# Kernel tuning notes

Hardware: AMD Instinct MI355X
Metric: run time of the kernel (lower is better)

## Reference

```python
import jax, jax.numpy as jnp
import numpy as np

PAD_Y = 16
PAD_X = 16


def setup_inputs() -> dict:
    key = jax.random.key(0)
    k1, k2, k3, k4 = jax.random.split(key, 4)
    B, NLAM, H, W = 4, 96, 256, 256
    KS = 15
    cube = jax.random.normal(k1, (B, NLAM, H, W), dtype=jnp.float32)
    # per-(ksequence, wavelength) dispersion shifts in pixels (a few px)
    dx = 3.0 * jax.random.normal(k2, (4, NLAM), dtype=jnp.float32)
    dy = 3.0 * jax.random.normal(k3, (4, NLAM), dtype=jnp.float32)
    psf = jax.random.uniform(k4, (KS, KS), dtype=jnp.float32)
    psf = psf / psf.sum()  # normalised PSF as in the original
    return {"cube": cube, "dx": dx, "dy": dy, "psf_kernel": psf}


def _forward(cube, dx, dy, psf_kernel):
    B, n_lam, H, W = cube.shape
    H_out, W_out = H + 2 * PAD_Y, W + 2 * PAD_X
    padded = jnp.pad(cube, ((0, 0), (0, 0), (PAD_Y, PAD_Y), (PAD_X, PAD_X)))
    yy, xx = jnp.meshgrid(jnp.arange(H_out, dtype=cube.dtype),
                          jnp.arange(W_out, dtype=cube.dtype), indexing="ij")

    def shift_one(img_b, d_x, d_y):
        # img_b: (B, H_out, W_out); output[y,x] = input[y-dy, x-dx], bilinear,
        # zeros outside (matches grid_sample padding_mode='zeros', align_corners=True)
        coords = jnp.stack([yy - d_y, xx - d_x])  # (2, H_out, W_out)
        return jax.vmap(lambda im: jax.scipy.ndimage.map_coordinates(
            im, coords, order=1, mode="constant", cval=0.0))(img_b)

    def per_k(dxk, dyk):
        # vmap over wavelengths -> (n_lam, B, H_out, W_out); accumulate over lambda
        shifted = jax.vmap(shift_one, in_axes=(1, 0, 0))(padded, dxk, dyk)
        return shifted.sum(0)  # (B, H_out, W_out)

    acc = jax.vmap(per_k)(dx, dy)            # (4, B, H_out, W_out)
    acc = jnp.transpose(acc, (1, 0, 2, 3))   # (B, 4, H_out, W_out)

    # PSF conv (same kernel every channel); conv is linear so conv(sum) == sum(conv)
    ks = psf_kernel.shape[-1]
    p = ks // 2
    x = acc.reshape(B * 4, 1, H_out, W_out)
    kern = psf_kernel.reshape(1, 1, ks, ks)
    out = jax.lax.conv_general_dilated(
        x, kern, window_strides=(1, 1), padding=[(p, p), (p, p)],
        dimension_numbers=("NCHW", "OIHW", "NCHW"))
    return out.reshape(B, 4, H_out, W_out)


def reference(cube, dx, dy, psf_kernel):
    return _forward(cube, dx, dy, psf_kernel)
```

## Files before the change

### kernel.cpp

```cpp
#include <hip/hip_runtime.h>

#define BB 4
#define NLAM 96
#define HH 256
#define WW 256
#define HO 288
#define WO 288
#define NK 4
#define KS 15
#define PADK 7

#define ACC_N ((size_t)BB * NK * HO * WO)

#define SP 105
#define SROWS 65
#define SQUADS 26

typedef float f4 __attribute__((ext_vector_type(4), aligned(4)));
typedef float f4a __attribute__((ext_vector_type(4)));

__global__ __launch_bounds__(384) void params_k(const float* __restrict__ dx,
                                                const float* __restrict__ dy,
                                                float4* __restrict__ pw,
                                                int2* __restrict__ po,
                                                int4* __restrict__ gmm) {
    __shared__ int sox[384], soy[384];
    const int i = threadIdx.x;
    const float sx = -dx[i] - 16.0f;
    const float sy = -dy[i] - 16.0f;
    const float fx = floorf(sx), fy = floorf(sy);
    const int ox = (int)fx, oy = (int)fy;
    po[i] = make_int2(ox, oy);
    pw[i] = make_float4(1.0f - (sx - fx), sx - fx, 1.0f - (sy - fy), sy - fy);
    sox[i] = ox; soy[i] = oy;
    __syncthreads();
    if (i < 64) {
        int mnx = sox[i], mxx = mnx, mny = soy[i], mxy = mny;
        for (int j = i + 64; j < 384; j += 64) {
            mnx = min(mnx, sox[j]); mxx = max(mxx, sox[j]);
            mny = min(mny, soy[j]); mxy = max(mxy, soy[j]);
        }
        for (int m = 32; m; m >>= 1) {
            mnx = min(mnx, __shfl_xor(mnx, m, 64));
            mxx = max(mxx, __shfl_xor(mxx, m, 64));
            mny = min(mny, __shfl_xor(mny, m, 64));
            mxy = max(mxy, __shfl_xor(mxy, m, 64));
        }
        if (i == 0) *gmm = make_int4(mnx, mxx, mny, mxy);
    }
}

__global__ __launch_bounds__(256, 4) void shift_accum(
        const float* __restrict__ cube,
        const float4* __restrict__ pw,
        const int2* __restrict__ po,
        const int4* __restrict__ gmm,
        float* __restrict__ part,
        int S, int chunk) {
    __shared__ float tile[SROWS * SP];
    const int zc  = blockIdx.z;
    const int b   = zc / S;
    const int c   = zc - b * S;
    const int tx0 = blockIdx.x * 64;
    const int ty0 = blockIdx.y * 32;
    const int tx  = threadIdx.x, ty = threadIdx.y;
    const int x   = tx0 + tx * 4;
    const int y   = ty0 + ty * 2;
    const int tid = ty * 16 + tx;
    const float* __restrict__ cb = cube + (size_t)b * NLAM * HH * WW;

    const int4 mm = *gmm;
    const int spanX = mm.y - mm.x;
    const int spanY = mm.w - mm.z;
    const bool lds_ok = (spanX <= 32) && (spanY <= 31);

    f4 a[NK][2];
#pragma unroll
    for (int k = 0; k < NK; ++k) { a[k][0] = (f4)0.f; a[k][1] = (f4)0.f; }

    const int l0 = min(NLAM, c * chunk);
    const int l1 = min(NLAM, l0 + chunk);

    if (lds_ok) {
        const int row0 = ty0 + mm.z;
        const int col0 = (tx0 + mm.x) & ~3;
        const int R    = spanY + 34;
        const int lrb  = ty * 2 - mm.z;
        const int lcb  = tx * 4 + (tx0 - col0);

        for (int lam = l0; lam < l1; ++lam) {
            const float* __restrict__ img = cb + lam * (HH * WW);
            for (int q = tid; q < R * SQUADS; q += 256) {
                const int r  = q / SQUADS;
                const int qi = q - r * SQUADS;
                const int gy = row0 + r;
                const int gc = col0 + qi * 4;
                f4a v = {0.f, 0.f, 0.f, 0.f};
                if ((unsigned)gy < (unsigned)HH) {
                    const float* rp = img + (gy << 8);
                    if ((unsigned)gc <= (unsigned)(WW - 4)) {
                        v = *(const f4a*)(rp + gc);
                    } else {
#pragma unroll
                        for (int e = 0; e < 4; ++e)
                            if ((unsigned)(gc + e) < (unsigned)WW) v[e] = rp[gc + e];
                    }
                }
                const int la = r * SP + qi * 4;
                tile[la]     = v.x; tile[la + 1] = v.y;
                tile[la + 2] = v.z; tile[la + 3] = v.w;
            }
            __syncthreads();
#pragma unroll
            for (int k = 0; k < NK; ++k) {
                const int i_ = k * NLAM + lam;
                const int2 o = po[i_]; const float4 w = pw[i_];
                const float* t = &tile[(lrb + o.y) * SP + (lcb + o.x)];
                float t0[5], t1[5], t2[5];
#pragma unroll
                for (int cc = 0; cc < 5; ++cc) {
                    t0[cc] = t[cc];
                    t1[cc] = t[SP + cc];
                    t2[cc] = t[2 * SP + cc];
                }
                float vb0[5], vb1[5];
#pragma unroll
                for (int cc = 0; cc < 5; ++cc) {
                    vb0[cc] = w.z * t0[cc] + w.w * t1[cc];
                    vb1[cc] = w.z * t1[cc] + w.w * t2[cc];
                }
                f4 d0, d1;
                d0.x = w.x * vb0[0] + w.y * vb0[1];
                d0.y = w.x * vb0[1] + w.y * vb0[2];
                d0.z = w.x * vb0[2] + w.y * vb0[3];
                d0.w = w.x * vb0[3] + w.y * vb0[4];
                d1.x = w.x * vb1[0] + w.y * vb1[1];
                d1.y = w.x * vb1[1] + w.y * vb1[2];
                d1.z = w.x * vb1[2] + w.y * vb1[3];
                d1.w = w.x * vb1[3] + w.y * vb1[4];
                a[k][0] += d0; a[k][1] += d1;
            }
            __syncthreads();
        }
    } else {
        for (int lam = l0; lam < l1; ++lam) {
            const float* __restrict__ img = cb + lam * (HH * WW);
#pragma unroll
            for (int k = 0; k < NK; ++k) {
                const int i_ = k * NLAM + lam;
                const int2 o = po[i_]; const float4 w = pw[i_];
#pragma unroll
                for (int j = 0; j < 2; ++j) {
                    const int iy = y + j + o.y;
                    const int ix = x + o.x;
                    const int cy0 = min(max(iy, 0), HH - 1);
                    const int cy1 = min(max(iy + 1, 0), HH - 1);
                    const float my0 = ((unsigned)iy       < (unsigned)HH) ? w.z : 0.0f;
                    const float my1 = ((unsigned)(iy + 1) < (unsigned)HH) ? w.w : 0.0f;
                    const float* r0p = img + cy0 * WW;
                    const float* r1p = img + cy1 * WW;
                    float rb[5];
#pragma unroll
                    for (int cc = 0; cc < 5; ++cc) {
                        const int cx = min(max(ix + cc, 0), WW - 1);
                        const float m = ((unsigned)(ix + cc) < (unsigned)WW) ? 1.0f : 0.0f;
                        rb[cc] = m * (my0 * r0p[cx] + my1 * r1p[cx]);
                    }
                    f4 d;
                    d.x = w.x * rb[0] + w.y * rb[1];
                    d.y = w.x * rb[1] + w.y * rb[2];
                    d.z = w.x * rb[2] + w.y * rb[3];
                    d.w = w.x * rb[3] + w.y * rb[4];
                    a[k][j] += d;
                }
            }
        }
    }

    if (x < WO) {
        const size_t hw = (size_t)HO * WO;
        float* pa = part + (size_t)c * ACC_N + ((size_t)(b * NK) * HO + y) * WO + x;
#pragma unroll
        for (int k = 0; k < NK; ++k) {
            *(f4a*)(pa + (size_t)k * hw)      = a[k][0];
            *(f4a*)(pa + (size_t)k * hw + WO) = a[k][1];
        }
    }
}

#define TPX 112
template <int S>
__global__ __launch_bounds__(192) void conv_psf(const float* __restrict__ part,
                                                const float* __restrict__ psf,
                                                float* __restrict__ out) {
    __shared__ float tilec[46][TPX];
    __shared__ float spsf[KS * KS];
    const int bk  = blockIdx.z;
    const int gx0 = blockIdx.x * 96 - PADK;
    const int gy0 = blockIdx.y * 32 - PADK;
    const float* __restrict__ ap = part + (size_t)bk * HO * WO;

    const int tid = threadIdx.y * 24 + threadIdx.x;
    for (int i = tid; i < KS * KS; i += 192) spsf[i] = psf[i];
    for (int i = tid; i < 46 * 110; i += 192) {
        int r = i / 110, c = i - r * 110;
        int gy = gy0 + r, gx = gx0 + c;
        float v = 0.f;
        if ((unsigned)gy < (unsigned)HO && (unsigned)gx < (unsigned)WO) {
            const size_t idx = (size_t)gy * WO + gx;
            float t[S];
#pragma unroll
            for (int cc = 0; cc < S; ++cc)
                t[cc] = ap[(size_t)cc * ACC_N + idx];
#pragma unroll
            for (int cc = 0; cc < S; ++cc) v += t[cc];
        }
        tilec[r][c] = v;
    }
    __syncthreads();

    const int x0 = threadIdx.x * 4;
    const int y0 = threadIdx.y * 4;
    float o[4][4] = {};

    for (int rr = 0; rr < 18; ++rr) {
        const float* rp = &tilec[y0 + rr][x0];
        float row[18];
#pragma unroll
        for (int q = 0; q < 4; ++q) {
            f4a v = *(const f4a*)(rp + 4 * q);
            row[4 * q]     = v.x; row[4 * q + 1] = v.y;
            row[4 * q + 2] = v.z; row[4 * q + 3] = v.w;
        }
        row[16] = rp[16]; row[17] = rp[17];

#pragma unroll
        for (int j = 0; j < 4; ++j) {
            const int ky = rr - j;
            if (ky >= 0 && ky < KS) {
                const float* w = &spsf[ky * KS];
#pragma unroll
                for (int kx = 0; kx < KS; ++kx) {
                    const float wv = w[kx];
#pragma unroll
                    for (int i = 0; i < 4; ++i) o[j][i] += wv * row[kx + i];
                }
            }
        }
    }

    const int xo = blockIdx.x * 96 + x0;
    const int yo = blockIdx.y * 32 + y0;
    float* op = out + ((size_t)bk * HO + yo) * WO + xo;
#pragma unroll
    for (int j = 0; j < 4; ++j) {
        f4a v = { o[j][0], o[j][1], o[j][2], o[j][3] };
        *(f4a*)(op + (size_t)j * WO) = v;
    }
}

extern "C" void kernel_launch(void* const* d_in, const int* in_sizes, int n_in,
                              void* d_out, int out_size, void* d_ws, size_t ws_size,
                              hipStream_t stream) {
    const float* cube = (const float*)d_in[0];
    const float* dx   = (const float*)d_in[1];
    const float* dy   = (const float*)d_in[2];
    const float* psf  = (const float*)d_in[3];
    float* out = (float*)d_out;

    const size_t ACCB   = ACC_N * sizeof(float);
    const size_t tables = 384 * sizeof(float4) + 384 * sizeof(int2) + sizeof(int4);

    int S = 1;
    for (int cand : {8, 6, 5, 4, 3, 2}) {
        if (ws_size >= (size_t)cand * ACCB + tables) { S = cand; break; }
    }
    const int chunk = (NLAM + S - 1) / S;

    float* part = (float*)d_ws;
    char*  tb   = (char*)d_ws + (size_t)S * ACCB;
    float4* pw  = (float4*)tb;
    int2*   po  = (int2*)(tb + 384 * sizeof(float4));
    int4*   gmm = (int4*)(tb + 384 * sizeof(float4) + 384 * sizeof(int2));

    params_k<<<1, 384, 0, stream>>>(dx, dy, pw, po, gmm);

    dim3 b1(16, 16);
    dim3 g1((WO + 63) / 64, HO / 32, BB * S);
    shift_accum<<<g1, b1, 0, stream>>>(cube, pw, po, gmm, part, S, chunk);

    dim3 b2(24, 8);
    dim3 g2(WO / 96, HO / 32, BB * NK);
    switch (S) {
        case 8: conv_psf<8><<<g2, b2, 0, stream>>>(part, psf, out); break;
        case 6: conv_psf<6><<<g2, b2, 0, stream>>>(part, psf, out); break;
        case 5: conv_psf<5><<<g2, b2, 0, stream>>>(part, psf, out); break;
        case 4: conv_psf<4><<<g2, b2, 0, stream>>>(part, psf, out); break;
        case 3: conv_psf<3><<<g2, b2, 0, stream>>>(part, psf, out); break;
        case 2: conv_psf<2><<<g2, b2, 0, stream>>>(part, psf, out); break;
        default: conv_psf<1><<<g2, b2, 0, stream>>>(part, psf, out); break;
    }
}
```

Before: 255.6 us.

## Precompute tile-load addresses, vectorize bilinear math, retile PSF conv, raise split count

The shift kernel now computes per-thread global offsets, masks and LDS addresses for the tile load once, outside the wavelength loop. Edge handling becomes branchless masked vector loads with a rare partial-quad fallback, and the bilinear blend uses packed float4 arithmetic. The conv kernel switches to 16-row tiles with 2 output rows per thread, vectorized reduction of the partials and padded PSF rows read as float4, and the wavelength split can now go up to 12 partial buffers. This aims to cut integer and address overhead and improve occupancy, at the cost of more registers and more partial-buffer traffic when S is larger.

Measured after the change: 226.7 us. -11.3%, faster.

```diff
diff --git a/kernel.cpp b/kernel.cpp
--- a/kernel.cpp
+++ b/kernel.cpp
@@ -13,8 +13,9 @@
 #define ACC_N ((size_t)BB * NK * HO * WO)
 
 #define SP 105
-#define SROWS 65
-#define SQUADS 26
+#define TILE_N (65 * SP)
+#define SDUMMY TILE_N
+#define NQ 7
 
 typedef float f4 __attribute__((ext_vector_type(4), aligned(4)));
 typedef float f4a __attribute__((ext_vector_type(4)));
@@ -57,7 +58,7 @@
         const int4* __restrict__ gmm,
         float* __restrict__ part,
         int S, int chunk) {
-    __shared__ float tile[SROWS * SP];
+    __shared__ float tile[TILE_N + 8];
     const int zc  = blockIdx.z;
     const int b   = zc / S;
     const int c   = zc - b * S;
@@ -74,9 +75,9 @@
     const int spanY = mm.w - mm.z;
     const bool lds_ok = (spanX <= 32) && (spanY <= 31);
 
-    f4 a[NK][2];
-#pragma unroll
-    for (int k = 0; k < NK; ++k) { a[k][0] = (f4)0.f; a[k][1] = (f4)0.f; }
+    f4a a[NK][2];
+#pragma unroll
+    for (int k = 0; k < NK; ++k) { a[k][0] = (f4a)0.f; a[k][1] = (f4a)0.f; }
 
     const int l0 = min(NLAM, c * chunk);
     const int l1 = min(NLAM, l0 + chunk);
@@ -85,37 +86,70 @@
         const int row0 = ty0 + mm.z;
         const int col0 = (tx0 + mm.x) & ~3;
         const int R    = spanY + 34;
-        const int lrb  = ty * 2 - mm.z;
-        const int lcb  = tx * 4 + (tx0 - col0);
+        const int tb0  = (ty * 2 - mm.z) * SP + (tx * 4 + (tx0 - col0));
+
+        int  goffB[NQ];
+        int  waddr[NQ];
+        float mf[NQ];
+        int  pf = 0;
+#pragma unroll
+        for (int s = 0; s < NQ; ++s) {
+            const int q  = tid + s * 256;
+            const bool inR = q < R * 26;
+            const int r  = q / 26;
+            const int qi = q - r * 26;
+            const int gy = row0 + r;
+            const int gc = col0 + qi * 4;
+            const bool rowOK = (unsigned)gy < (unsigned)HH;
+            const bool fullQ = rowOK && gc >= 0 && gc <= WW - 4;
+            const bool partQ = inR && rowOK && !fullQ && (gc + 3 >= 0) && (gc < WW);
+            const int gyc = min(max(gy, 0), HH - 1);
+            const int gcc = min(max(gc, 0), WW - 4);
+            goffB[s] = (gyc * WW + gcc) * 4;
+            mf[s]    = (inR && fullQ) ? 1.0f : 0.0f;
+            waddr[s] = (inR && !partQ) ? (r * SP + qi * 4) : SDUMMY;
+            if (partQ) pf |= 1 << s;
+        }
+
+        for (int i = tid; i < TILE_N + 8; i += 256) tile[i] = 0.0f;
+        __syncthreads();
 
         for (int lam = l0; lam < l1; ++lam) {
-            const float* __restrict__ img = cb + lam * (HH * WW);
-            for (int q = tid; q < R * SQUADS; q += 256) {
-                const int r  = q / SQUADS;
-                const int qi = q - r * SQUADS;
-                const int gy = row0 + r;
-                const int gc = col0 + qi * 4;
-                f4a v = {0.f, 0.f, 0.f, 0.f};
-                if ((unsigned)gy < (unsigned)HH) {
-                    const float* rp = img + (gy << 8);
-                    if ((unsigned)gc <= (unsigned)(WW - 4)) {
-                        v = *(const f4a*)(rp + gc);
-                    } else {
+            const char* __restrict__ ib = (const char*)(cb + lam * (HH * WW));
+#pragma unroll
+            for (int s = 0; s < NQ; ++s) {
+                f4a v = *(const f4a*)(ib + goffB[s]);
+                const float m = mf[s];
+                const int wa = waddr[s];
+                tile[wa]     = v.x * m;
+                tile[wa + 1] = v.y * m;
+                tile[wa + 2] = v.z * m;
+                tile[wa + 3] = v.w * m;
+            }
+            if (pf) {
+#pragma unroll
+                for (int s = 0; s < NQ; ++s) {
+                    if (pf & (1 << s)) {
+                        const int q  = tid + s * 256;
+                        const int r  = q / 26;
+                        const int qi = q - r * 26;
+                        const int gy = row0 + r;
+                        const int gc = col0 + qi * 4;
+                        const float* rp = (const float*)ib + gy * WW;
+                        const int la = r * SP + qi * 4;
 #pragma unroll
                         for (int e = 0; e < 4; ++e)
-                            if ((unsigned)(gc + e) < (unsigned)WW) v[e] = rp[gc + e];
+                            if ((unsigned)(gc + e) < (unsigned)WW)
+                                tile[la + e] = rp[gc + e];
                     }
                 }
-                const int la = r * SP + qi * 4;
-                tile[la]     = v.x; tile[la + 1] = v.y;
-                tile[la + 2] = v.z; tile[la + 3] = v.w;
             }
             __syncthreads();
 #pragma unroll
             for (int k = 0; k < NK; ++k) {
                 const int i_ = k * NLAM + lam;
                 const int2 o = po[i_]; const float4 w = pw[i_];
-                const float* t = &tile[(lrb + o.y) * SP + (lcb + o.x)];
+                const float* t = tile + tb0 + o.y * SP + o.x;
                 float t0[5], t1[5], t2[5];
 #pragma unroll
                 for (int cc = 0; cc < 5; ++cc) {
@@ -123,22 +157,17 @@
                     t1[cc] = t[SP + cc];
                     t2[cc] = t[2 * SP + cc];
                 }
-                float vb0[5], vb1[5];
-#pragma unroll
-                for (int cc = 0; cc < 5; ++cc) {
-                    vb0[cc] = w.z * t0[cc] + w.w * t1[cc];
-                    vb1[cc] = w.z * t1[cc] + w.w * t2[cc];
-                }
-                f4 d0, d1;
-                d0.x = w.x * vb0[0] + w.y * vb0[1];
-                d0.y = w.x * vb0[1] + w.y * vb0[2];
-                d0.z = w.x * vb0[2] + w.y * vb0[3];
-                d0.w = w.x * vb0[3] + w.y * vb0[4];
-                d1.x = w.x * vb1[0] + w.y * vb1[1];
-                d1.y = w.x * vb1[1] + w.y * vb1[2];
-                d1.z = w.x * vb1[2] + w.y * vb1[3];
-                d1.w = w.x * vb1[3] + w.y * vb1[4];
-                a[k][0] += d0; a[k][1] += d1;
+                f4a r0 = {t0[0], t0[1], t0[2], t0[3]};
+                f4a r1 = {t1[0], t1[1], t1[2], t1[3]};
+                f4a r2 = {t2[0], t2[1], t2[2], t2[3]};
+                f4a vb0 = w.z * r0 + w.w * r1;
+                f4a vb1 = w.z * r1 + w.w * r2;
+                const float e0 = w.z * t0[4] + w.w * t1[4];
+                const float e1 = w.z * t1[4] + w.w * t2[4];
+                f4a s0 = {vb0.y, vb0.z, vb0.w, e0};
+                f4a s1 = {vb1.y, vb1.z, vb1.w, e1};
+                a[k][0] += w.x * vb0 + w.y * s0;
+                a[k][1] += w.x * vb1 + w.y * s1;
             }
             __syncthreads();
         }
@@ -166,7 +195,7 @@
                         const float m = ((unsigned)(ix + cc) < (unsigned)WW) ? 1.0f : 0.0f;
                         rb[cc] = m * (my0 * r0p[cx] + my1 * r1p[cx]);
                     }
-                    f4 d;
+                    f4a d;
                     d.x = w.x * rb[0] + w.y * rb[1];
                     d.y = w.x * rb[1] + w.y * rb[2];
                     d.z = w.x * rb[2] + w.y * rb[3];
@@ -188,43 +217,74 @@
     }
 }
 
-#define TPX 112
+#define CPX 112
+#define CROWS 30
+#define CTILE_N (CROWS * CPX)
+#define CDUMMY CTILE_N
+#define NQC 5
+
 template <int S>
 __global__ __launch_bounds__(192) void conv_psf(const float* __restrict__ part,
                                                 const float* __restrict__ psf,
                                                 float* __restrict__ out) {
-    __shared__ float tilec[46][TPX];
-    __shared__ float spsf[KS * KS];
+    __shared__ float tilec[CTILE_N + 8];
+    __shared__ float spsf[KS][16];
     const int bk  = blockIdx.z;
     const int gx0 = blockIdx.x * 96 - PADK;
-    const int gy0 = blockIdx.y * 32 - PADK;
+    const int gy0 = blockIdx.y * 16 - PADK;
     const float* __restrict__ ap = part + (size_t)bk * HO * WO;
 
     const int tid = threadIdx.y * 24 + threadIdx.x;
-    for (int i = tid; i < KS * KS; i += 192) spsf[i] = psf[i];
-    for (int i = tid; i < 46 * 110; i += 192) {
-        int r = i / 110, c = i - r * 110;
-        int gy = gy0 + r, gx = gx0 + c;
-        float v = 0.f;
-        if ((unsigned)gy < (unsigned)HO && (unsigned)gx < (unsigned)WO) {
-            const size_t idx = (size_t)gy * WO + gx;
-            float t[S];
-#pragma unroll
-            for (int cc = 0; cc < S; ++cc)
-                t[cc] = ap[(size_t)cc * ACC_N + idx];
-#pragma unroll
-            for (int cc = 0; cc < S; ++cc) v += t[cc];
-        }
-        tilec[r][c] = v;
+    for (int i = tid; i < KS * 16; i += 192) {
+        const int r = i >> 4, cc2 = i & 15;
+        spsf[r][cc2] = (cc2 < KS) ? psf[r * KS + cc2] : 0.0f;
+    }
+
+    int goffB[NQC], laddr[NQC];
+    f4a cmask[NQC];
+#pragma unroll
+    for (int s = 0; s < NQC; ++s) {
+        const int q  = tid + s * 192;
+        const bool inR = q < CROWS * 28;
+        const int r  = q / 28;
+        const int qi = q - r * 28;
+        const int gy = gy0 + r;
+        const int gx = gx0 + qi * 4;
+        const bool rowOK = (unsigned)gy < (unsigned)HO;
+        const int gyc = min(max(gy, 0), HO - 1);
+        goffB[s] = (gyc * WO + gx) * 4;
+        laddr[s] = inR ? (r * CPX + qi * 4) : CDUMMY;
+        f4a m;
+#pragma unroll
+        for (int e = 0; e < 4; ++e)
+            m[e] = (inR && rowOK && (unsigned)(gx + e) < (unsigned)WO) ? 1.0f : 0.0f;
+        cmask[s] = m;
+    }
+
+#pragma unroll
+    for (int s = 0; s < NQC; ++s) {
+        const char* base = (const char*)ap + goffB[s];
+        f4a acc = (f4a)0.f;
+#pragma unroll
+        for (int cc = 0; cc < S; ++cc) {
+            f4 v = *(const f4*)(base + (size_t)cc * (ACC_N * 4));
+            acc += (f4a)v;
+        }
+        acc *= cmask[s];
+        const int la = laddr[s];
+        tilec[la] = acc.x; tilec[la + 1] = acc.y;
+        tilec[la + 2] = acc.z; tilec[la + 3] = acc.w;
     }
     __syncthreads();
 
     const int x0 = threadIdx.x * 4;
-    const int y0 = threadIdx.y * 4;
-    float o[4][4] = {};
-
-    for (int rr = 0; rr < 18; ++rr) {
-        const float* rp = &tilec[y0 + rr][x0];
+    const int y0 = threadIdx.y * 2;
+    f4a o0 = (f4a)0.f, o1 = (f4a)0.f;
+    f4a prev0, prev1, prev2, prev3;
+
+#pragma unroll
+    for (int rr = 0; rr < 16; ++rr) {
+        const float* rp = &tilec[(y0 + rr) * CPX + x0];
         float row[18];
 #pragma unroll
         for (int q = 0; q < 4; ++q) {
@@ -234,29 +294,39 @@
         }
         row[16] = rp[16]; row[17] = rp[17];
 
-#pragma unroll
-        for (int j = 0; j < 4; ++j) {
-            const int ky = rr - j;
-            if (ky >= 0 && ky < KS) {
-                const float* w = &spsf[ky * KS];
-#pragma unroll
-                for (int kx = 0; kx < KS; ++kx) {
-                    const float wv = w[kx];
-#pragma unroll
-                    for (int i = 0; i < 4; ++i) o[j][i] += wv * row[kx + i];
-                }
-            }
-        }
+        f4a c0, c1, c2, c3;
+        if (rr < 15) {
+            c0 = *(const f4a*)&spsf[rr][0];
+            c1 = *(const f4a*)&spsf[rr][4];
+            c2 = *(const f4a*)&spsf[rr][8];
+            c3 = *(const f4a*)&spsf[rr][12];
+        }
+        if (rr < 15) {
+#pragma unroll
+            for (int kx = 0; kx < KS; ++kx) {
+                const float wv = (kx < 4) ? c0[kx] : (kx < 8) ? c1[kx - 4]
+                               : (kx < 12) ? c2[kx - 8] : c3[kx - 12];
+                f4a rv = {row[kx], row[kx + 1], row[kx + 2], row[kx + 3]};
+                o0 += wv * rv;
+            }
+        }
+        if (rr >= 1) {
+#pragma unroll
+            for (int kx = 0; kx < KS; ++kx) {
+                const float wv = (kx < 4) ? prev0[kx] : (kx < 8) ? prev1[kx - 4]
+                               : (kx < 12) ? prev2[kx - 8] : prev3[kx - 12];
+                f4a rv = {row[kx], row[kx + 1], row[kx + 2], row[kx + 3]};
+                o1 += wv * rv;
+            }
+        }
+        prev0 = c0; prev1 = c1; prev2 = c2; prev3 = c3;
     }
 
     const int xo = blockIdx.x * 96 + x0;
-    const int yo = blockIdx.y * 32 + y0;
+    const int yo = blockIdx.y * 16 + y0;
     float* op = out + ((size_t)bk * HO + yo) * WO + xo;
-#pragma unroll
-    for (int j = 0; j < 4; ++j) {
-        f4a v = { o[j][0], o[j][1], o[j][2], o[j][3] };
-        *(f4a*)(op + (size_t)j * WO) = v;
-    }
+    *(f4a*)op        = o0;
+    *(f4a*)(op + WO) = o1;
 }
 
 extern "C" void kernel_launch(void* const* d_in, const int* in_sizes, int n_in,
@@ -272,13 +342,13 @@
     const size_t tables = 384 * sizeof(float4) + 384 * sizeof(int2) + sizeof(int4);
 
     int S = 1;
-    for (int cand : {8, 6, 5, 4, 3, 2}) {
-        if (ws_size >= (size_t)cand * ACCB + tables) { S = cand; break; }
+    for (int cand : {12, 8, 6, 4, 3, 2}) {
+        if (ws_size >= 64 + (size_t)cand * ACCB + tables + 4096) { S = cand; break; }
     }
     const int chunk = (NLAM + S - 1) / S;
 
-    float* part = (float*)d_ws;
-    char*  tb   = (char*)d_ws + (size_t)S * ACCB;
+    float* part = (float*)((char*)d_ws + 64);
+    char*  tb   = (char*)part + (size_t)S * ACCB;
     float4* pw  = (float4*)tb;
     int2*   po  = (int2*)(tb + 384 * sizeof(float4));
     int4*   gmm = (int4*)(tb + 384 * sizeof(float4) + 384 * sizeof(int2));
@@ -290,14 +360,14 @@
     shift_accum<<<g1, b1, 0, stream>>>(cube, pw, po, gmm, part, S, chunk);
 
     dim3 b2(24, 8);
-    dim3 g2(WO / 96, HO / 32, BB * NK);
+    dim3 g2(WO / 96, HO / 16, BB * NK);
     switch (S) {
-        case 8: conv_psf<8><<<g2, b2, 0, stream>>>(part, psf, out); break;
-        case 6: conv_psf<6><<<g2, b2, 0, stream>>>(part, psf, out); break;
-        case 5: conv_psf<5><<<g2, b2, 0, stream>>>(part, psf, out); break;
-        case 4: conv_psf<4><<<g2, b2, 0, stream>>>(part, psf, out); break;
-        case 3: conv_psf<3><<<g2, b2, 0, stream>>>(part, psf, out); break;
-        case 2: conv_psf<2><<<g2, b2, 0, stream>>>(part, psf, out); break;
+        case 12: conv_psf<12><<<g2, b2, 0, stream>>>(part, psf, out); break;
+        case 8:  conv_psf<8><<<g2, b2, 0, stream>>>(part, psf, out); break;
+        case 6:  conv_psf<6><<<g2, b2, 0, stream>>>(part, psf, out); break;
+        case 4:  conv_psf<4><<<g2, b2, 0, stream>>>(part, psf, out); break;
+        case 3:  conv_psf<3><<<g2, b2, 0, stream>>>(part, psf, out); break;
+        case 2:  conv_psf<2><<<g2, b2, 0, stream>>>(part, psf, out); break;
         default: conv_psf<1><<<g2, b2, 0, stream>>>(part, psf, out); break;
     }
 }
```
